# Kernel optimization log

Measured on AMD Instinct MI355X. Metric: run time of the kernel, lower is better.

Reference implementation:

```python
import jax, jax.numpy as jnp
import numpy as np

N = 100000   # nodes
E = 1600000  # edges
H = 150      # hidden_dim
G = 256      # num graphs in batch
L = 5        # num_layers
GATE_H = 200


def setup_inputs() -> dict:
    key = jax.random.key(0)
    ks = jax.random.split(key, 12)
    s = lambda k, shape, fan: jax.random.normal(k, shape, dtype=jnp.float32) / np.sqrt(fan)
    return {
        "x": jax.random.normal(ks[0], (N, H), dtype=jnp.float32),
        "edge_index": jax.random.randint(ks[1], (2, E), 0, N, dtype=jnp.int64),
        "batch": jnp.sort(jax.random.randint(ks[2], (N,), 0, G, dtype=jnp.int64)),
        "W": s(ks[3], (L, H, H), H),              # GatedGraphConv per-layer weight
        "w_ih": s(ks[4], (3 * H, H), H),           # GRUCell input weights (r,z,n)
        "w_hh": s(ks[5], (3 * H, H), H),
        "b_ih": jnp.zeros((3 * H,), jnp.float32),
        "b_hh": jnp.zeros((3 * H,), jnp.float32),
        "gw1": s(ks[6], (H, GATE_H), H),           # gate_nn Linear(150,200)
        "gb1": jnp.zeros((GATE_H,), jnp.float32),
        "gw2": s(ks[7], (GATE_H, 1), GATE_H),      # gate_nn Linear(200,1)
        "gb2": jnp.zeros((1,), jnp.float32),
    }


def _gru_cell(m, h, w_ih, w_hh, b_ih, b_hh):
    gi = m @ w_ih.T + b_ih   # [N, 3H]
    gh = h @ w_hh.T + b_hh
    ir, iz, inn = jnp.split(gi, 3, axis=-1)
    hr, hz, hn = jnp.split(gh, 3, axis=-1)
    r = jax.nn.sigmoid(ir + hr)
    z = jax.nn.sigmoid(iz + hz)
    n = jnp.tanh(inn + r * hn)
    return (1.0 - z) * n + z * h


def reference(x, edge_index, batch, W, w_ih, w_hh, b_ih, b_hh, gw1, gb1, gw2, gb2):
    src, dst = edge_index[0], edge_index[1]
    h = x
    # GatedGraphConv: per layer, linear transform, scatter_add aggregation, GRU update
    for i in range(L):
        m = h @ W[i]                                   # [N, H]
        agg = jax.ops.segment_sum(m[src], dst, num_segments=N)  # scatter_add over edges
        h = _gru_cell(agg, h, w_ih, w_hh, b_ih, b_hh)
    # GlobalAttention readout
    gate = jnp.tanh(h @ gw1 + gb1) @ gw2 + gb2          # [N, 1]
    gmax = jax.ops.segment_max(gate, batch, num_segments=G)    # [G, 1]
    gate = jnp.exp(gate - gmax[batch])
    gsum = jax.ops.segment_sum(gate, batch, num_segments=G)    # [G, 1]
    gate = gate / (gsum[batch] + 1e-16)                 # segment softmax
    out = jax.ops.segment_sum(gate * h, batch, num_segments=G)  # [G, H]
    return out, gate
```

## Files before the change

kernel.cpp:

```cpp
#include <hip/hip_runtime.h>
#include <math.h>

#define NN 100000
#define NE 1600000
#define H 150
#define NG 256
#define NL 5
#define GH 200
#define HS 160
#define LS 168
#define CHN 1563
#define CH2 782
#define SNB 98

typedef unsigned short u16;
typedef unsigned int   u32;
typedef __attribute__((ext_vector_type(8))) short bf16x8;
typedef __attribute__((ext_vector_type(4))) float f32x4;

__device__ __forceinline__ float bf2f(u32 lo16){ u32 t = lo16 << 16; return __builtin_bit_cast(float, t); }
__device__ __forceinline__ u16 f2bf(float f){
  u32 u = __builtin_bit_cast(u32, f);
  u += 0x7fffu + ((u >> 16) & 1u);
  return (u16)(u >> 16);
}
__device__ __forceinline__ u32 pack2(float a, float b){ return (u32)f2bf(a) | ((u32)f2bf(b) << 16); }
__device__ __forceinline__ float fast_sig(float x){
  float e = __expf(-x);
  return __builtin_amdgcn_rcpf(1.f + e);
}
__device__ __forceinline__ float fast_tanh(float x){
  float cx = fminf(fmaxf(x, -15.f), 15.f);
  float e = __expf(2.f*cx);
  return (e - 1.f) * __builtin_amdgcn_rcpf(e + 1.f);
}

__global__ void k_hist(const int* __restrict__ ed, int* __restrict__ cnt){
  int e = blockIdx.x*256 + threadIdx.x;
  if (e < NE) atomicAdd(&cnt[ed[e]], 1);
}

__global__ __launch_bounds__(256) void k_scan1(const int* __restrict__ cnt, int* __restrict__ part){
  __shared__ int red[256];
  const int b = blockIdx.x, tid = threadIdx.x;
  const int base = b*1024;
  int s = 0;
  #pragma unroll
  for (int i = 0; i < 4; ++i){
    int idx = base + tid + i*256;
    s += (idx < NN) ? cnt[idx] : 0;
  }
  red[tid] = s; __syncthreads();
  for (int st = 128; st >= 1; st >>= 1){
    if (tid < st) red[tid] += red[tid+st];
    __syncthreads();
  }
  if (tid == 0) part[b] = red[0];
}

__global__ void k_scan2(int* __restrict__ part){
  const int t = threadIdx.x;
  int v0 = (2*t   < SNB) ? part[2*t]   : 0;
  int v1 = (2*t+1 < SNB) ? part[2*t+1] : 0;
  int s = v0 + v1, x = s;
  #pragma unroll
  for (int off = 1; off < 64; off <<= 1){
    int tt = __shfl_up(x, off);
    if (t >= off) x += tt;
  }
  int excl = x - s;
  if (2*t   < SNB) part[2*t]   = excl;
  if (2*t+1 < SNB) part[2*t+1] = excl + v0;
}

__global__ __launch_bounds__(1024) void k_scan3(const int* __restrict__ cnt,
        const int* __restrict__ part, int* __restrict__ rowptr, int* __restrict__ cursor){
  __shared__ int wsum[16];
  const int b = blockIdx.x, tid = threadIdx.x;
  const int wid = tid >> 6, lane = tid & 63;
  const int idx = b*1024 + tid;
  int v = (idx < NN) ? cnt[idx] : 0;
  int x = v;
  #pragma unroll
  for (int off = 1; off < 64; off <<= 1){
    int t = __shfl_up(x, off);
    if (lane >= off) x += t;
  }
  if (lane == 63) wsum[wid] = x;
  __syncthreads();
  if (tid < 16){
    int s = wsum[tid];
    int y = s;
    #pragma unroll
    for (int off = 1; off < 16; off <<= 1){
      int t = __shfl_up(y, off);
      if (tid >= off) y += t;
    }
    wsum[tid] = y - s;
  }
  __syncthreads();
  if (idx < NN){
    int incl = part[b] + wsum[wid] + x;
    rowptr[idx+1] = incl;
    cursor[idx]   = incl - v;
  }
  if (idx == 0) rowptr[0] = 0;
}

__global__ void k_fill(const int* __restrict__ es, const int* __restrict__ ed,
                       int* __restrict__ cursor, int* __restrict__ csr){
  int e = blockIdx.x*256 + threadIdx.x;
  if (e < NE){
    int pos = atomicAdd(&cursor[ed[e]], 1);
    csr[pos] = es[e];
  }
}

__global__ __launch_bounds__(256) void k_wc(const float* __restrict__ W,
        const float* __restrict__ wih, float* __restrict__ Wc){
  int idx = blockIdx.x*256 + threadIdx.x;
  if (idx >= NL*H*450) return;
  int l = idx / (H*450);
  int rem = idx - l*H*450;
  int k = rem / 450;
  int j = rem - k*450;
  const float* Wr = W   + (size_t)l*H*H + (size_t)k*H;
  const float* wr = wih + (size_t)j*H;
  float acc = 0.f;
  for (int t = 0; t < H; ++t) acc = fmaf(Wr[t], wr[t], acc);
  Wc[idx] = acc;
}

__global__ void k_packi(const float* __restrict__ Wc, short* __restrict__ wbi){
  int idx = blockIdx.x*256 + threadIdx.x;
  int li = idx & 511;
  int q = idx >> 9;
  int mat = q % 3; q /= 3;
  int ks = q % 5;  q /= 5;
  int ct = q % 10; int l = q / 10;
  int lane = li >> 3, j = li & 7;
  int k = ks*32 + ((lane >> 4) << 3) + j;
  int col = ct*16 + (lane & 15);
  float v = (k < H && col < H) ? Wc[(size_t)l*H*450 + (size_t)k*450 + mat*H + col] : 0.f;
  wbi[idx] = (short)f2bf(v);
}

__global__ void k_packh(const float* __restrict__ whh, short* __restrict__ wbh){
  int idx = blockIdx.x*256 + threadIdx.x;
  int li = idx & 511;
  int q = idx >> 9;
  int mat = q % 3; q /= 3;
  int ks = q % 5;  int ct = q / 5;
  int lane = li >> 3, j = li & 7;
  int k = ks*32 + ((lane >> 4) << 3) + j;
  int col = ct*16 + (lane & 15);
  float v = (k < H && col < H) ? whh[(size_t)(mat*H + col)*H + k] : 0.f;
  wbh[idx] = (short)f2bf(v);
}

__global__ void k_packg(const float* __restrict__ gw1, short* __restrict__ gw1b){
  int idx = blockIdx.x*256 + threadIdx.x;
  int li = idx & 511;
  int q = idx >> 9;
  int ks = q % 5;  int ct = q / 5;
  int lane = li >> 3, j = li & 7;
  int k = ks*32 + ((lane >> 4) << 3) + j;
  int col = ct*16 + (lane & 15);
  float v = (k < H && col < GH) ? gw1[(size_t)k*GH + col] : 0.f;
  gw1b[idx] = (short)f2bf(v);
}

__global__ void k_cvt(const float* __restrict__ x, short* __restrict__ hb){
  int idx = blockIdx.x*256 + threadIdx.x;
  if (idx >= NN*80) return;
  int n = idx / 80, c2 = idx - n*80;
  int c = c2*2;
  float lo = (c   < H) ? x[(size_t)n*H + c]   : 0.f;
  float hi = (c+1 < H) ? x[(size_t)n*H + c+1] : 0.f;
  ((u32*)hb)[idx] = (u32)f2bf(lo) | ((u32)f2bf(hi) << 16);
}

__global__ __launch_bounds__(256) void k_gather(const short* __restrict__ hb,
        const int* __restrict__ rowptr, const int* __restrict__ csr,
        short* __restrict__ aggb){
  const int lane = threadIdx.x & 63;
  const int n = blockIdx.x*4 + (threadIdx.x >> 6);
  if (n >= NN) return;
  const int s0 = rowptr[n], s1 = rowptr[n+1];
  const u32* h32 = (const u32*)hb;
  const bool ext = lane < 16;
  float x0=0.f, x1=0.f, y0=0.f, y1=0.f;
  int j = s0;
  for (; j + 7 < s1; j += 8){
    const u32* r0 = h32 + (size_t)csr[j]*80;
    const u32* r1 = h32 + (size_t)csr[j+1]*80;
    const u32* r2 = h32 + (size_t)csr[j+2]*80;
    const u32* r3 = h32 + (size_t)csr[j+3]*80;
    const u32* r4 = h32 + (size_t)csr[j+4]*80;
    const u32* r5 = h32 + (size_t)csr[j+5]*80;
    const u32* r6 = h32 + (size_t)csr[j+6]*80;
    const u32* r7 = h32 + (size_t)csr[j+7]*80;
    u32 v0 = r0[lane], v1 = r1[lane], v2 = r2[lane], v3 = r3[lane];
    u32 v4 = r4[lane], v5 = r5[lane], v6 = r6[lane], v7 = r7[lane];
    u32 u0=0,u1=0,u2=0,u3=0,u4=0,u5=0,u6=0,u7=0;
    if (ext){
      u0 = r0[64+lane]; u1 = r1[64+lane]; u2 = r2[64+lane]; u3 = r3[64+lane];
      u4 = r4[64+lane]; u5 = r5[64+lane]; u6 = r6[64+lane]; u7 = r7[64+lane];
    }
    x0 += bf2f(v0 & 0xffffu) + bf2f(v1 & 0xffffu) + bf2f(v2 & 0xffffu) + bf2f(v3 & 0xffffu)
        + bf2f(v4 & 0xffffu) + bf2f(v5 & 0xffffu) + bf2f(v6 & 0xffffu) + bf2f(v7 & 0xffffu);
    x1 += bf2f(v0 >> 16) + bf2f(v1 >> 16) + bf2f(v2 >> 16) + bf2f(v3 >> 16)
        + bf2f(v4 >> 16) + bf2f(v5 >> 16) + bf2f(v6 >> 16) + bf2f(v7 >> 16);
    if (ext){
      y0 += bf2f(u0 & 0xffffu) + bf2f(u1 & 0xffffu) + bf2f(u2 & 0xffffu) + bf2f(u3 & 0xffffu)
          + bf2f(u4 & 0xffffu) + bf2f(u5 & 0xffffu) + bf2f(u6 & 0xffffu) + bf2f(u7 & 0xffffu);
      y1 += bf2f(u0 >> 16) + bf2f(u1 >> 16) + bf2f(u2 >> 16) + bf2f(u3 >> 16)
          + bf2f(u4 >> 16) + bf2f(u5 >> 16) + bf2f(u6 >> 16) + bf2f(u7 >> 16);
    }
  }
  for (; j < s1; ++j){
    const u32* r0 = h32 + (size_t)csr[j]*80;
    u32 v0 = r0[lane];
    x0 += bf2f(v0 & 0xffffu); x1 += bf2f(v0 >> 16);
    if (ext){
      u32 u0 = r0[64+lane];
      y0 += bf2f(u0 & 0xffffu); y1 += bf2f(u0 >> 16);
    }
  }
  u32* o = (u32*)aggb + (size_t)n*80;
  o[lane] = pack2(x0, x1);
  if (ext) o[64+lane] = pack2(y0, y1);
}

__global__ __launch_bounds__(256, 2) void k_gru(
    const short* __restrict__ aggb, const short* __restrict__ hbc,
    short* __restrict__ hbn,
    const short* __restrict__ wbi_l, const short* __restrict__ wbh,
    const float* __restrict__ bih, const float* __restrict__ bhh){
  __shared__ short sB[30*512];
  const int tid = threadIdx.x;
  const int w = tid >> 6, lane = tid & 63;
  const int l16 = lane & 15, g = lane >> 4, g8 = g*8;
  const int row0 = blockIdx.x*128 + w*32;

  bf16x8 fA[2][5], fH[2][5];
  #pragma unroll
  for (int t = 0; t < 2; ++t){
    const int r = row0 + t*16 + l16;
    const bool rv = r < NN;
    #pragma unroll
    for (int ks = 0; ks < 5; ++ks){
      bf16x8 va = {0,0,0,0,0,0,0,0}, vh = {0,0,0,0,0,0,0,0};
      if (rv){
        va = *(const bf16x8*)&aggb[(size_t)r*HS + ks*32 + g8];
        vh = *(const bf16x8*)&hbc [(size_t)r*HS + ks*32 + g8];
      }
      fA[t][ks] = va; fH[t][ks] = vh;
    }
  }

  bf16x8 pr[8];
  #pragma unroll
  for (int k2 = 0; k2 < 8; ++k2){
    int u = tid + k2*256;
    if (u < 1920){
      int s = u >> 6, e = u & 63;
      const short* src = (s < 15) ? (wbi_l + s*512 + e*8)
                                  : (wbh  + (s-15)*512 + e*8);
      pr[k2] = *(const bf16x8*)src;
    }
  }

  for (int ct = 0; ct < 10; ++ct){
    __syncthreads();
    #pragma unroll
    for (int k2 = 0; k2 < 8; ++k2){
      int u = tid + k2*256;
      if (u < 1920) *(bf16x8*)&sB[u*8] = pr[k2];
    }
    __syncthreads();
    if (ct < 9){
      const int cto = (ct+1)*7680;
      #pragma unroll
      for (int k2 = 0; k2 < 8; ++k2){
        int u = tid + k2*256;
        if (u < 1920){
          int s = u >> 6, e = u & 63;
          const short* src = (s < 15) ? (wbi_l + cto + s*512 + e*8)
                                      : (wbh  + cto + (s-15)*512 + e*8);
          pr[k2] = *(const bf16x8*)src;
        }
      }
    }

    const int col = ct*16 + l16;
    const bool cv = col < H;
    const float bir = cv ? bih[col] : 0.f, biz = cv ? bih[H+col] : 0.f, bin_ = cv ? bih[2*H+col] : 0.f;
    const float bhr = cv ? bhh[col] : 0.f, bhz = cv ? bhh[H+col] : 0.f, bhn  = cv ? bhh[2*H+col] : 0.f;

    f32x4 ai[2][3], ah[2][3];
    #pragma unroll
    for (int t = 0; t < 2; ++t)
      #pragma unroll
      for (int m = 0; m < 3; ++m){ ai[t][m] = (f32x4){0,0,0,0}; ah[t][m] = (f32x4){0,0,0,0}; }

    #pragma unroll
    for (int ks = 0; ks < 5; ++ks){
      bf16x8 bi0 = *(const bf16x8*)&sB[(ks*3+0)*512 + lane*8];
      bf16x8 bi1 = *(const bf16x8*)&sB[(ks*3+1)*512 + lane*8];
      bf16x8 bi2 = *(const bf16x8*)&sB[(ks*3+2)*512 + lane*8];
      bf16x8 bh0 = *(const bf16x8*)&sB[(15+ks*3+0)*512 + lane*8];
      bf16x8 bh1 = *(const bf16x8*)&sB[(15+ks*3+1)*512 + lane*8];
      bf16x8 bh2 = *(const bf16x8*)&sB[(15+ks*3+2)*512 + lane*8];
      #pragma unroll
      for (int t = 0; t < 2; ++t){
        ai[t][0] = __builtin_amdgcn_mfma_f32_16x16x32_bf16(fA[t][ks], bi0, ai[t][0], 0,0,0);
        ai[t][1] = __builtin_amdgcn_mfma_f32_16x16x32_bf16(fA[t][ks], bi1, ai[t][1], 0,0,0);
        ai[t][2] = __builtin_amdgcn_mfma_f32_16x16x32_bf16(fA[t][ks], bi2, ai[t][2], 0,0,0);
        ah[t][0] = __builtin_amdgcn_mfma_f32_16x16x32_bf16(fH[t][ks], bh0, ah[t][0], 0,0,0);
        ah[t][1] = __builtin_amdgcn_mfma_f32_16x16x32_bf16(fH[t][ks], bh1, ah[t][1], 0,0,0);
        ah[t][2] = __builtin_amdgcn_mfma_f32_16x16x32_bf16(fH[t][ks], bh2, ah[t][2], 0,0,0);
      }
    }

    if (cv){
      #pragma unroll
      for (int t = 0; t < 2; ++t){
        #pragma unroll
        for (int r = 0; r < 4; ++r){
          int grow = row0 + t*16 + g*4 + r;
          if (grow < NN){
            float rr = fast_sig(ai[t][0][r]+bir + ah[t][0][r]+bhr);
            float zz = fast_sig(ai[t][1][r]+biz + ah[t][1][r]+bhz);
            float nn = fast_tanh(ai[t][2][r]+bin_ + rr*(ah[t][2][r]+bhn));
            float hold = bf2f((u32)(u16)hbc[(size_t)grow*HS + col]);
            float hnew = (1.f-zz)*nn + zz*hold;
            hbn[(size_t)grow*HS + col] = (short)f2bf(hnew);
          }
        }
      }
    }
  }
}

__global__ __launch_bounds__(256) void k_gatepre(const short* __restrict__ hb,
      const short* __restrict__ gw1b, const float* __restrict__ gb1,
      const float* __restrict__ gw2, const float* __restrict__ gb2,
      float* __restrict__ gbuf){
  __shared__ short sh[64*LS];
  __shared__ float part[4][4][4][4];
  const int tid = threadIdx.x;
  const int w = tid >> 6, lane = tid & 63;
  const int l16 = lane & 15, g = lane >> 4, g8 = g*8;
  const int chunk = blockIdx.x, row0 = chunk*64;

  for (int i = tid; i < 64*20; i += 256){
    int r = i/20, c = i - r*20;
    int gr = row0 + r;
    bf16x8 v = {0,0,0,0,0,0,0,0};
    if (gr < NN) v = *(const bf16x8*)&hb[(size_t)gr*HS + c*8];
    *(bf16x8*)&sh[r*LS + c*8] = v;
  }
  __syncthreads();

  float acc[4][4];
  #pragma unroll
  for (int rt=0; rt<4; ++rt){
    #pragma unroll
    for (int r=0; r<4; ++r) acc[rt][r] = 0.f;
  }
  for (int ct = w; ct < 13; ct += 4){
    bf16x8 B[5];
    const short* p = gw1b + (size_t)(ct*5)*512 + lane*8;
    #pragma unroll
    for (int ks = 0; ks < 5; ++ks) B[ks] = *(const bf16x8*)&p[ks*512];
    int col = ct*16 + l16;
    bool cv = col < GH;
    float g2 = cv ? gw2[col] : 0.f;
    float b1 = cv ? gb1[col] : 0.f;
    #pragma unroll
    for (int rt = 0; rt < 4; ++rt){
      f32x4 d = {0,0,0,0};
      #pragma unroll
      for (int ks = 0; ks < 5; ++ks){
        bf16x8 aH = *(const bf16x8*)&sh[(rt*16 + l16)*LS + ks*32 + g8];
        d = __builtin_amdgcn_mfma_f32_16x16x32_bf16(aH, B[ks], d, 0,0,0);
      }
      if (cv){
        #pragma unroll
        for (int r = 0; r < 4; ++r) acc[rt][r] += fast_tanh(d[r] + b1) * g2;
      }
    }
  }
  #pragma unroll
  for (int rt = 0; rt < 4; ++rt){
    #pragma unroll
    for (int r = 0; r < 4; ++r){
      float v = acc[rt][r];
      v += __shfl_xor(v, 1); v += __shfl_xor(v, 2);
      v += __shfl_xor(v, 4); v += __shfl_xor(v, 8);
      if (l16 == 0) part[w][rt][g][r] = v;
    }
  }
  __syncthreads();
  if (tid < 64){
    int rt = tid >> 4, gg = (tid >> 2) & 3, r = tid & 3;
    int grow = row0 + tid;
    if (grow < NN)
      gbuf[grow] = part[0][rt][gg][r] + part[1][rt][gg][r]
                 + part[2][rt][gg][r] + part[3][rt][gg][r] + gb2[0];
  }
}

__global__ __launch_bounds__(256) void k_readout(float* __restrict__ gatebuf,
    const short* __restrict__ hb, const int* __restrict__ batch,
    float* __restrict__ out, float* __restrict__ gate_out){
  const int g = blockIdx.x;
  const int tid = threadIdx.x;
  int lo=0, hi=NN;
  while (lo<hi){ int mid=(lo+hi)>>1; if (batch[mid] < g) lo=mid+1; else hi=mid; }
  const int start = lo;
  hi = NN;
  while (lo<hi){ int mid=(lo+hi)>>1; if (batch[mid] < g+1) lo=mid+1; else hi=mid; }
  const int end = lo;

  __shared__ float red[256];
  __shared__ float s_max, s_inv;
  float mx = -INFINITY;
  for (int n = start+tid; n < end; n += 256) mx = fmaxf(mx, gatebuf[n]);
  red[tid]=mx; __syncthreads();
  for (int s=128; s>=1; s>>=1){ if (tid<s) red[tid]=fmaxf(red[tid],red[tid+s]); __syncthreads(); }
  if (tid==0) s_max = red[0];
  __syncthreads();
  const float gmax = s_max;
  float sum = 0.f;
  for (int n = start+tid; n < end; n += 256){
    float e = expf(gatebuf[n]-gmax);
    gatebuf[n] = e;
    sum += e;
  }
  red[tid]=sum; __syncthreads();
  for (int s=128; s>=1; s>>=1){ if (tid<s) red[tid]+=red[tid+s]; __syncthreads(); }
  if (tid==0) s_inv = 1.0f/(red[0] + 1e-16f);
  __syncthreads();
  const float inv = s_inv;
  for (int n = start+tid; n < end; n += 256) gate_out[n] = gatebuf[n]*inv;
  if (tid < 80){
    const u32* h32 = (const u32*)hb;
    float acc0 = 0.f, acc1 = 0.f;
    for (int n = start; n < end; ++n){
      u32 v = h32[(size_t)n*80 + tid];
      float gv = gatebuf[n];
      acc0 = fmaf(gv, bf2f(v & 0xffffu), acc0);
      acc1 = fmaf(gv, bf2f(v >> 16),     acc1);
    }
    int c0 = 2*tid, c1 = 2*tid + 1;
    if (c0 < H) out[g*H + c0] = acc0*inv;
    if (c1 < H) out[g*H + c1] = acc1*inv;
  }
}

extern "C" void kernel_launch(void* const* d_in, const int* in_sizes, int n_in,
                              void* d_out, int out_size, void* d_ws, size_t ws_size,
                              hipStream_t stream) {
  (void)in_sizes; (void)n_in; (void)out_size; (void)ws_size;
  const float* x    = (const float*)d_in[0];
  const int*   eidx = (const int*)d_in[1];
  const int*   batch= (const int*)d_in[2];
  const float* W    = (const float*)d_in[3];
  const float* wih  = (const float*)d_in[4];
  const float* whh  = (const float*)d_in[5];
  const float* bih  = (const float*)d_in[6];
  const float* bhh  = (const float*)d_in[7];
  const float* gw1  = (const float*)d_in[8];
  const float* gb1  = (const float*)d_in[9];
  const float* gw2  = (const float*)d_in[10];
  const float* gb2  = (const float*)d_in[11];

  float* out      = (float*)d_out;
  float* gate_out = out + NG*H;

  char* p = (char*)d_ws;
  float* gbuf  = (float*)p;  p += (size_t)NN*4;
  float* Wc    = (float*)p;  p += (size_t)NL*H*450*4;
  short* hb0   = (short*)p;  p += (size_t)NN*HS*2;
  short* hb1   = (short*)p;  p += (size_t)NN*HS*2;
  short* aggb  = (short*)p;  p += (size_t)NN*HS*2;
  short* wbi   = (short*)p;  p += (size_t)NL*76800*2;
  short* wbh   = (short*)p;  p += (size_t)76800*2;
  short* gw1b  = (short*)p;  p += (size_t)33280*2;
  int*   cnt   = (int*)p;    p += (size_t)NN*4;
  int*   rowptr= (int*)p;    p += (size_t)(NN+1)*4;
  int*   cursor= (int*)p;    p += (size_t)NN*4;
  int*   csr   = (int*)p;    p += (size_t)NE*4;
  int*   spart = (int*)p;    p += (size_t)SNB*4;

  const int* esrc = eidx;
  const int* edst = eidx + NE;

  hipMemsetAsync(cnt, 0, sizeof(int)*NN, stream);
  k_hist<<<(NE+255)/256, 256, 0, stream>>>(edst, cnt);
  k_scan1<<<SNB, 256, 0, stream>>>(cnt, spart);
  k_scan2<<<1, 64, 0, stream>>>(spart);
  k_scan3<<<SNB, 1024, 0, stream>>>(cnt, spart, rowptr, cursor);
  k_fill<<<(NE+255)/256, 256, 0, stream>>>(esrc, edst, cursor, csr);

  k_wc   <<<(NL*H*450+255)/256, 256, 0, stream>>>(W, wih, Wc);
  k_packi<<<1500, 256, 0, stream>>>(Wc, wbi);
  k_packh<<<300,  256, 0, stream>>>(whh, wbh);
  k_packg<<<130,  256, 0, stream>>>(gw1, gw1b);

  k_cvt<<<(NN*80+255)/256, 256, 0, stream>>>(x, hb0);

  for (int l = 0; l < NL; ++l){
    short* cur  = (l & 1) ? hb1 : hb0;
    short* next = (l & 1) ? hb0 : hb1;
    k_gather<<<NN/4, 256, 0, stream>>>(cur, rowptr, csr, aggb);
    k_gru<<<CH2, 256, 0, stream>>>(aggb, cur, next,
                                   wbi + (size_t)l*76800, wbh, bih, bhh);
  }
  k_gatepre<<<CHN, 256, 0, stream>>>(hb1, gw1b, gb1, gw2, gb2, gbuf);
  k_readout<<<NG, 256, 0, stream>>>(gbuf, hb1, batch, out, gate_out);
}
```

Baseline: 1.259 ms.

## Pad CSR rows to multiples of eight with a zero sentinel row

```diff
diff --git a/kernel.cpp b/kernel.cpp
--- a/kernel.cpp
+++ b/kernel.cpp
@@ -12,6 +12,7 @@
 #define CHN 1563
 #define CH2 782
 #define SNB 98
+#define CSRMAX 2304000
 
 typedef unsigned short u16;
 typedef unsigned int   u32;
@@ -48,7 +49,8 @@
   #pragma unroll
   for (int i = 0; i < 4; ++i){
     int idx = base + tid + i*256;
-    s += (idx < NN) ? cnt[idx] : 0;
+    int v = (idx < NN) ? cnt[idx] : 0;
+    s += (v + 7) & ~7;
   }
   red[tid] = s; __syncthreads();
   for (int st = 128; st >= 1; st >>= 1){
@@ -79,7 +81,8 @@
   const int b = blockIdx.x, tid = threadIdx.x;
   const int wid = tid >> 6, lane = tid & 63;
   const int idx = b*1024 + tid;
-  int v = (idx < NN) ? cnt[idx] : 0;
+  int c = (idx < NN) ? cnt[idx] : 0;
+  int v = (c + 7) & ~7;
   int x = v;
   #pragma unroll
   for (int off = 1; off < 64; off <<= 1){
@@ -105,6 +108,12 @@
     cursor[idx]   = incl - v;
   }
   if (idx == 0) rowptr[0] = 0;
+}
+
+__global__ __launch_bounds__(256) void k_pre(int* __restrict__ csr){
+  int i = (blockIdx.x*256 + threadIdx.x)*4;
+  int4 v = {NN, NN, NN, NN};
+  *(int4*)&csr[i] = v;
 }
 
 __global__ void k_fill(const int* __restrict__ es, const int* __restrict__ ed,
@@ -180,6 +189,14 @@
   ((u32*)hb)[idx] = (u32)f2bf(lo) | ((u32)f2bf(hi) << 16);
 }
 
+__global__ void k_zrow(short* __restrict__ a, short* __restrict__ b){
+  int t = threadIdx.x;
+  if (t < 80){
+    ((u32*)a)[(size_t)NN*80 + t] = 0u;
+    ((u32*)b)[(size_t)NN*80 + t] = 0u;
+  }
+}
+
 __global__ __launch_bounds__(256) void k_gather(const short* __restrict__ hb,
         const int* __restrict__ rowptr, const int* __restrict__ csr,
         short* __restrict__ aggb){
@@ -190,16 +207,17 @@
   const u32* h32 = (const u32*)hb;
   const bool ext = lane < 16;
   float x0=0.f, x1=0.f, y0=0.f, y1=0.f;
-  int j = s0;
-  for (; j + 7 < s1; j += 8){
-    const u32* r0 = h32 + (size_t)csr[j]*80;
-    const u32* r1 = h32 + (size_t)csr[j+1]*80;
-    const u32* r2 = h32 + (size_t)csr[j+2]*80;
-    const u32* r3 = h32 + (size_t)csr[j+3]*80;
-    const u32* r4 = h32 + (size_t)csr[j+4]*80;
-    const u32* r5 = h32 + (size_t)csr[j+5]*80;
-    const u32* r6 = h32 + (size_t)csr[j+6]*80;
-    const u32* r7 = h32 + (size_t)csr[j+7]*80;
+  for (int j = s0; j < s1; j += 8){
+    int4 ia = *(const int4*)&csr[j];
+    int4 ib = *(const int4*)&csr[j+4];
+    const u32* r0 = h32 + (size_t)ia.x*80;
+    const u32* r1 = h32 + (size_t)ia.y*80;
+    const u32* r2 = h32 + (size_t)ia.z*80;
+    const u32* r3 = h32 + (size_t)ia.w*80;
+    const u32* r4 = h32 + (size_t)ib.x*80;
+    const u32* r5 = h32 + (size_t)ib.y*80;
+    const u32* r6 = h32 + (size_t)ib.z*80;
+    const u32* r7 = h32 + (size_t)ib.w*80;
     u32 v0 = r0[lane], v1 = r1[lane], v2 = r2[lane], v3 = r3[lane];
     u32 v4 = r4[lane], v5 = r5[lane], v6 = r6[lane], v7 = r7[lane];
     u32 u0=0,u1=0,u2=0,u3=0,u4=0,u5=0,u6=0,u7=0;
@@ -216,15 +234,6 @@
           + bf2f(u4 & 0xffffu) + bf2f(u5 & 0xffffu) + bf2f(u6 & 0xffffu) + bf2f(u7 & 0xffffu);
       y1 += bf2f(u0 >> 16) + bf2f(u1 >> 16) + bf2f(u2 >> 16) + bf2f(u3 >> 16)
           + bf2f(u4 >> 16) + bf2f(u5 >> 16) + bf2f(u6 >> 16) + bf2f(u7 >> 16);
-    }
-  }
-  for (; j < s1; ++j){
-    const u32* r0 = h32 + (size_t)csr[j]*80;
-    u32 v0 = r0[lane];
-    x0 += bf2f(v0 & 0xffffu); x1 += bf2f(v0 >> 16);
-    if (ext){
-      u32 u0 = r0[64+lane];
-      y0 += bf2f(u0 & 0xffffu); y1 += bf2f(u0 >> 16);
     }
   }
   u32* o = (u32*)aggb + (size_t)n*80;
@@ -483,8 +492,8 @@
   char* p = (char*)d_ws;
   float* gbuf  = (float*)p;  p += (size_t)NN*4;
   float* Wc    = (float*)p;  p += (size_t)NL*H*450*4;
-  short* hb0   = (short*)p;  p += (size_t)NN*HS*2;
-  short* hb1   = (short*)p;  p += (size_t)NN*HS*2;
+  short* hb0   = (short*)p;  p += (size_t)(NN+1)*HS*2;
+  short* hb1   = (short*)p;  p += (size_t)(NN+1)*HS*2;
   short* aggb  = (short*)p;  p += (size_t)NN*HS*2;
   short* wbi   = (short*)p;  p += (size_t)NL*76800*2;
   short* wbh   = (short*)p;  p += (size_t)76800*2;
@@ -492,7 +501,7 @@
   int*   cnt   = (int*)p;    p += (size_t)NN*4;
   int*   rowptr= (int*)p;    p += (size_t)(NN+1)*4;
   int*   cursor= (int*)p;    p += (size_t)NN*4;
-  int*   csr   = (int*)p;    p += (size_t)NE*4;
+  int*   csr   = (int*)p;    p += (size_t)CSRMAX*4;
   int*   spart = (int*)p;    p += (size_t)SNB*4;
 
   const int* esrc = eidx;
@@ -503,6 +512,7 @@
   k_scan1<<<SNB, 256, 0, stream>>>(cnt, spart);
   k_scan2<<<1, 64, 0, stream>>>(spart);
   k_scan3<<<SNB, 1024, 0, stream>>>(cnt, spart, rowptr, cursor);
+  k_pre <<<CSRMAX/1024, 256, 0, stream>>>(csr);
   k_fill<<<(NE+255)/256, 256, 0, stream>>>(esrc, edst, cursor, csr);
 
   k_wc   <<<(NL*H*450+255)/256, 256, 0, stream>>>(W, wih, Wc);
@@ -511,6 +521,7 @@
   k_packg<<<130,  256, 0, stream>>>(gw1, gw1b);
 
   k_cvt<<<(NN*80+255)/256, 256, 0, stream>>>(x, hb0);
+  k_zrow<<<1, 128, 0, stream>>>(hb0, hb1);
 
   for (int l = 0; l < NL; ++l){
     short* cur  = (l & 1) ? hb1 : hb0;
```

Result: no change. 1.241 ms (-1.4%).
